# Optimization experiments

Measured on AMD Instinct MI355X. Metric: run time of the kernel, lower is better.

Reference implementation:

```python
import jax, jax.numpy as jnp
import numpy as np


def setup_inputs() -> dict:
    key = jax.random.key(0)
    ks = jax.random.split(key, 8)
    B, T, DIM = 4096, 64, 16
    H1, H2, LAT = 256, 256, 64
    KD = DIM + LAT  # Koopman dim = 80
    x = jax.random.normal(ks[0], (B, T, DIM), dtype=jnp.float32)
    # Encoder: Linear(16->256, bias), Linear(256->256, bias), Linear(256->64, no bias)
    W1 = jax.random.normal(ks[1], (H1, DIM), dtype=jnp.float32) / np.sqrt(DIM)
    b1 = jnp.zeros((H1,), dtype=jnp.float32)
    W2 = jax.random.normal(ks[2], (H2, H1), dtype=jnp.float32) / np.sqrt(H1)
    b2 = jnp.zeros((H2,), dtype=jnp.float32)
    W3 = jax.random.normal(ks[3], (LAT, H2), dtype=jnp.float32) / np.sqrt(H2)
    # Koopman operator, scaled for stable 63-step rollout
    K = jax.random.normal(ks[4], (KD, KD), dtype=jnp.float32) * (0.9 / np.sqrt(KD))
    return {"x": x, "W1": W1, "b1": b1, "W2": W2, "b2": b2, "W3": W3,
            "K": K, "n_shifts": 64}


def reference(x, W1, b1, W2, b2, W3, K, n_shifts):
    # x: [B, T, dim]; slice to n_shifts steps
    x = x[:, :n_shifts, :]
    # Encoder MLP (relu on all but last layer; last layer bias-free, dropout p=0)
    h = jax.nn.relu(jnp.einsum('btd,hd->bth', x, W1) + b1)
    h = jax.nn.relu(jnp.einsum('bth,gh->btg', h, W2) + b2)
    g = jnp.einsum('btg,lg->btl', h, W3)
    y = jnp.concatenate([x, g], axis=-1)  # [B, T, dim+lat]
    # Linear recurrence: y_{n+1} = y_n @ K^T, starting from y[:, 0]
    y0 = y[:, 0, :]  # [B, KD]

    def step(carry, _):
        nxt = carry @ K.T
        return nxt, nxt

    _, rest = jax.lax.scan(step, y0, None, length=n_shifts - 1)  # [T-1, B, KD]
    y_pred = jnp.concatenate([y0[:, None, :], jnp.swapaxes(rest, 0, 1)], axis=1)
    return y, y_pred
```

## Files before the change

### kernel.cpp

```cpp
#include <hip/hip_runtime.h>
#include <hip/hip_bf16.h>

#define NB   4096
#define NT   64
#define NDIM 16
#define NH1  256
#define NH2  256
#define NLAT 64
#define NKD  80
#define YROW (NT * NKD)
#define KTAB 98304
#define KSLOT 15360

#define FROW 184
#define FIMG_B (80 * FROW * 2)

typedef __attribute__((ext_vector_type(8))) short bf16x8;
typedef __attribute__((ext_vector_type(4))) float f32x4;

#define MFMA __builtin_amdgcn_mfma_f32_16x16x32_bf16

static __device__ __forceinline__ short f2bf(float f) {
  union { float f; unsigned u; } v; v.f = f;
  unsigned r = v.u + 0x7fffu + ((v.u >> 16) & 1u);
  return (short)(r >> 16);
}
static __device__ __forceinline__ float bf2f(short h) {
  union { unsigned u; float f; } v; v.u = ((unsigned)(unsigned short)h) << 16;
  return v.f;
}
static __device__ __forceinline__ bf16x8 pack8(float4 a, float4 b) {
  bf16x8 r;
  r[0] = f2bf(a.x); r[1] = f2bf(a.y); r[2] = f2bf(a.z); r[3] = f2bf(a.w);
  r[4] = f2bf(b.x); r[5] = f2bf(b.y); r[6] = f2bf(b.z); r[7] = f2bf(b.w);
  return r;
}
static __device__ __forceinline__ void split8(float4 v0, float4 v1, bf16x8& h, bf16x8& l) {
  h = pack8(v0, v1);
  float4 r0, r1;
  r0.x = v0.x - bf2f(h[0]); r0.y = v0.y - bf2f(h[1]);
  r0.z = v0.z - bf2f(h[2]); r0.w = v0.w - bf2f(h[3]);
  r1.x = v1.x - bf2f(h[4]); r1.y = v1.y - bf2f(h[5]);
  r1.z = v1.z - bf2f(h[6]); r1.w = v1.w - bf2f(h[7]);
  l = pack8(r0, r1);
}

__global__ __launch_bounds__(256) void prep_kernel(const float* __restrict__ W1,
                                                   const float* __restrict__ W2,
                                                   const float* __restrict__ W3,
                                                   short* __restrict__ ws) {
  int i = blockIdx.x * 256 + threadIdx.x;
  {
    int e = i & 7, l = (i >> 3) & 63, nt = (i >> 9) & 15, kk = i >> 13;
    int g = nt * 16 + (l & 15);
    int h = kk * 32 + (l >> 4) * 8 + e;
    ws[i] = f2bf(W2[g * NH1 + h]);
  }
  if (i < 16384) {
    int e = i & 7, l = (i >> 3) & 63, nt = (i >> 9) & 3, kk = i >> 11;
    int g = nt * 16 + (l & 15);
    int h = kk * 32 + (l >> 4) * 8 + e;
    ws[65536 + i] = f2bf(W3[g * NH2 + h]);
  }
  if (i < 8192) {
    int e = i & 7, l = (i >> 3) & 63, nt = i >> 9;
    int g = nt * 16 + (l & 15);
    int k = (l >> 4) * 8 + e;
    ws[81920 + i] = (k < NDIM) ? f2bf(W1[g * NDIM + k]) : (short)0;
  }
}

__global__ void kpow_kernel(const float* __restrict__ Kg, short* __restrict__ ws) {
  extern __shared__ char smem[];
  short* kA   = (short*)smem;
  short* curA = (short*)(smem + FIMG_B);
  short* curB = (short*)(smem + 2 * FIMG_B);
  short* nxtA = (short*)(smem + 3 * FIMG_B);
  short* nxtB = (short*)(smem + 4 * FIMG_B);

  const int tid  = threadIdx.x;
  const int lane = tid & 63;
  const int w    = tid >> 6;
  const int l15  = lane & 15;
  const int kg   = lane >> 4;
  const int t    = blockIdx.x + 1;

  for (int i = tid; i < 6400; i += 512) {
    float v = Kg[i];
    int r = i / 80, c = i - r * 80;
    short hi = f2bf(v);
    short lo = f2bf(v - bf2f(hi));
    kA[r * FROW + c] = hi;        kA[r * FROW + 96 + c] = lo;
    curA[r * FROW + c] = hi;      curA[r * FROW + 96 + c] = lo;
    curB[c * FROW + r] = hi;      curB[c * FROW + 96 + r] = lo;
  }
  __syncthreads();

  auto mm = [&](const short* Ai, const short* Bi, short* DA, short* DB) {
    for (int id = w; id < 25; id += 8) {
      const int mt = id / 5, nt = id % 5;
      f32x4 acc = {0.f, 0.f, 0.f, 0.f};
#pragma unroll
      for (int kk = 0; kk < 3; ++kk) {
        const int k0 = kk * 32 + kg * 8;
        bf16x8 ah = {}, al = {}, bh = {}, bl = {};
        if (k0 < 80) {
          const short* ap = Ai + (mt * 16 + l15) * FROW + k0;
          const short* bp = Bi + (nt * 16 + l15) * FROW + k0;
          ah = *(const bf16x8*)ap;  al = *(const bf16x8*)(ap + 96);
          bh = *(const bf16x8*)bp;  bl = *(const bf16x8*)(bp + 96);
        }
        acc = MFMA(ah, bh, acc, 0, 0, 0);
        acc = MFMA(al, bh, acc, 0, 0, 0);
        acc = MFMA(ah, bl, acc, 0, 0, 0);
      }
      const int n = nt * 16 + l15;
      const int rowb = mt * 16 + kg * 4;
      short4 hs, ls;
#pragma unroll
      for (int r = 0; r < 4; ++r) {
        float v = acc[r];
        short hi = f2bf(v);
        short lo = f2bf(v - bf2f(hi));
        DA[(rowb + r) * FROW + n] = hi;
        DA[(rowb + r) * FROW + 96 + n] = lo;
        ((short*)&hs)[r] = hi;
        ((short*)&ls)[r] = lo;
      }
      *(short4*)(DB + n * FROW + rowb) = hs;
      *(short4*)(DB + n * FROW + 96 + rowb) = ls;
    }
    __syncthreads();
  };

  const int h = 31 - __clz(t);
  for (int bit = h - 1; bit >= 0; --bit) {
    mm(curA, curB, nxtA, nxtB);
    { short* p;
      p = curA; curA = nxtA; nxtA = p;
      p = curB; curB = nxtB; nxtB = p; }
    if ((t >> bit) & 1) {
      mm(kA, curB, nxtA, nxtB);
      { short* p;
        p = curA; curA = nxtA; nxtA = p;
        p = curB; curB = nxtB; nxtB = p; }
    }
  }

  short* kt = ws + KTAB + t * KSLOT;
  for (int s = tid; s < 960; s += 512) {
    int f = s >> 6, ln = s & 63;
    int kk = f / 5, nt = f % 5;
    int k0 = kk * 32 + (ln >> 4) * 8;
    int n  = nt * 16 + (ln & 15);
    bf16x8 h8 = {}, l8 = {};
    if (k0 < 80) {
      const short* ap = curA + n * FROW + k0;
      h8 = *(const bf16x8*)ap;
      l8 = *(const bf16x8*)(ap + 96);
    }
    *(bf16x8*)(kt + f * 512 + ln * 8) = h8;
    *(bf16x8*)(kt + 7680 + f * 512 + ln * 8) = l8;
  }
}

__global__ __launch_bounds__(256, 4) void mlp_kernel(const float* __restrict__ x,
                                                     const float* __restrict__ b1g,
                                                     const float* __restrict__ b2g,
                                                     const short* __restrict__ ws,
                                                     float* __restrict__ y) {
  extern __shared__ char smem[];
  short* h1s = (short*)smem;

  const int tid  = threadIdx.x;
  const int lane = tid & 63;
  const int w    = tid >> 6;
  const int l15  = lane & 15;
  const int kg   = lane >> 4;
  const long b   = blockIdx.x;

  const short* W2f = ws;
  const short* W3f = ws + 65536;
  const short* W1f = ws + 81920;

  const float4 xv = ((const float4*)(x + b * 1024))[tid];

  bf16x8 xf[4];
#pragma unroll
  for (int j = 0; j < 4; ++j) {
    const int tok = j * 16 + l15;
    bf16x8 f = {};
    if (kg < 2) {
      const float4* p = (const float4*)(x + (b * 64 + tok) * 16 + kg * 8);
      f = pack8(p[0], p[1]);
    }
    xf[j] = f;
  }

#pragma unroll
  for (int i = 0; i < 4; ++i) {
    const int mt = w * 4 + i;
    const bf16x8 wa = *(const bf16x8*)(W1f + (mt * 64 + lane) * 8);
    const float4 bias = *(const float4*)(b1g + mt * 16 + kg * 4);
#pragma unroll
    for (int j = 0; j < 4; ++j) {
      f32x4 c = {0.f, 0.f, 0.f, 0.f};
      c = MFMA(wa, xf[j], c, 0, 0, 0);
      const int tok = j * 16 + l15;
      float v0 = c[0] + bias.x; v0 = v0 > 0.f ? v0 : 0.f;
      float v1 = c[1] + bias.y; v1 = v1 > 0.f ? v1 : 0.f;
      float v2 = c[2] + bias.z; v2 = v2 > 0.f ? v2 : 0.f;
      float v3 = c[3] + bias.w; v3 = v3 > 0.f ? v3 : 0.f;
      short4 st = {f2bf(v0), f2bf(v1), f2bf(v2), f2bf(v3)};
      *(short4*)(h1s + tok * 264 + mt * 16 + kg * 4) = st;
    }
  }
  __syncthreads();

  f32x4 acc2[4][4];
#pragma unroll
  for (int i = 0; i < 4; ++i)
#pragma unroll
    for (int j = 0; j < 4; ++j) acc2[i][j] = (f32x4){0.f, 0.f, 0.f, 0.f};

#pragma unroll 2
  for (int kk = 0; kk < 8; ++kk) {
    bf16x8 wa[4], hb[4];
#pragma unroll
    for (int i = 0; i < 4; ++i)
      wa[i] = *(const bf16x8*)(W2f + ((kk * 16 + w * 4 + i) * 64 + lane) * 8);
#pragma unroll
    for (int j = 0; j < 4; ++j)
      hb[j] = *(const bf16x8*)(h1s + (j * 16 + l15) * 264 + kk * 32 + kg * 8);
#pragma unroll
    for (int i = 0; i < 4; ++i)
#pragma unroll
      for (int j = 0; j < 4; ++j)
        acc2[i][j] = MFMA(wa[i], hb[j], acc2[i][j], 0, 0, 0);
  }
  __syncthreads();

#pragma unroll
  for (int i = 0; i < 4; ++i) {
    const int mt = w * 4 + i;
    const float4 bias = *(const float4*)(b2g + mt * 16 + kg * 4);
#pragma unroll
    for (int j = 0; j < 4; ++j) {
      const int tok = j * 16 + l15;
      float v0 = acc2[i][j][0] + bias.x; v0 = v0 > 0.f ? v0 : 0.f;
      float v1 = acc2[i][j][1] + bias.y; v1 = v1 > 0.f ? v1 : 0.f;
      float v2 = acc2[i][j][2] + bias.z; v2 = v2 > 0.f ? v2 : 0.f;
      float v3 = acc2[i][j][3] + bias.w; v3 = v3 > 0.f ? v3 : 0.f;
      short4 st = {f2bf(v0), f2bf(v1), f2bf(v2), f2bf(v3)};
      *(short4*)(h1s + tok * 264 + mt * 16 + kg * 4) = st;
    }
  }
  __syncthreads();

  f32x4 acc3[4];
#pragma unroll
  for (int j = 0; j < 4; ++j) acc3[j] = (f32x4){0.f, 0.f, 0.f, 0.f};
#pragma unroll 2
  for (int kk = 0; kk < 8; ++kk) {
    const bf16x8 wa = *(const bf16x8*)(W3f + ((kk * 4 + w) * 64 + lane) * 8);
#pragma unroll
    for (int j = 0; j < 4; ++j) {
      const bf16x8 hb =
          *(const bf16x8*)(h1s + (j * 16 + l15) * 264 + kk * 32 + kg * 8);
      acc3[j] = MFMA(wa, hb, acc3[j], 0, 0, 0);
    }
  }

  *(float4*)(y + (b * 64 + (tid >> 2)) * 80 + (tid & 3) * 4) = xv;
#pragma unroll
  for (int j = 0; j < 4; ++j) {
    const int tok = j * 16 + l15;
    *(float4*)(y + (b * 64 + tok) * 80 + 16 + w * 16 + kg * 4) =
        *(float4*)&acc3[j];
  }
}

__global__ __launch_bounds__(512, 4) void ypred_kernel(const short* __restrict__ ws,
                                                       const float* __restrict__ y,
                                                       float* __restrict__ yp) {
  const int tid  = threadIdx.x;
  const int lane = tid & 63;
  const int w    = tid >> 6;
  const int m16  = lane & 15;
  const int kg   = lane >> 4;
  const int bc   = blockIdx.x & 15;
  const int t    = blockIdx.x >> 4;
  const long b0  = (long)bc * 256;

  if (t == 0) {
    for (int i = tid; i < 5120; i += 512) {
      int r = i / 20, q = (i % 20) * 4;
      *(float4*)(yp + (b0 + r) * YROW + q) = *(const float4*)(y + (b0 + r) * YROW + q);
    }
    return;
  }

  bf16x8 ah[2][3], al[2][3];
#pragma unroll
  for (int m = 0; m < 2; ++m) {
#pragma unroll
    for (int kk = 0; kk < 3; ++kk) {
      const int k0 = kk * 32 + kg * 8;
      bf16x8 fh = {}, fl = {};
      if (k0 < 80) {
        const float4* p =
            (const float4*)(y + (b0 + (2 * w + m) * 16 + m16) * YROW + k0);
        split8(p[0], p[1], fh, fl);
      }
      ah[m][kk] = fh;
      al[m][kk] = fl;
    }
  }

  const short* kt = ws + KTAB + t * KSLOT;
  f32x4 acc[2][5];
#pragma unroll
  for (int m = 0; m < 2; ++m)
#pragma unroll
    for (int nt = 0; nt < 5; ++nt) acc[m][nt] = (f32x4){0.f, 0.f, 0.f, 0.f};

#pragma unroll
  for (int kk = 0; kk < 3; ++kk) {
#pragma unroll
    for (int nt = 0; nt < 5; ++nt) {
      const bf16x8 bh = *(const bf16x8*)(kt + ((kk * 5 + nt) * 64 + lane) * 8);
      const bf16x8 bl = *(const bf16x8*)(kt + 7680 + ((kk * 5 + nt) * 64 + lane) * 8);
#pragma unroll
      for (int m = 0; m < 2; ++m) {
        acc[m][nt] = MFMA(ah[m][kk], bh, acc[m][nt], 0, 0, 0);
        acc[m][nt] = MFMA(al[m][kk], bh, acc[m][nt], 0, 0, 0);
        acc[m][nt] = MFMA(ah[m][kk], bl, acc[m][nt], 0, 0, 0);
      }
    }
  }
#pragma unroll
  for (int m = 0; m < 2; ++m)
#pragma unroll
    for (int nt = 0; nt < 5; ++nt)
#pragma unroll
      for (int r = 0; r < 4; ++r)
        yp[(b0 + (2 * w + m) * 16 + kg * 4 + r) * YROW + (long)t * 80 + nt * 16 + m16] =
            acc[m][nt][r];
}

extern "C" void kernel_launch(void* const* d_in, const int* in_sizes, int n_in,
                              void* d_out, int out_size, void* d_ws, size_t ws_size,
                              hipStream_t stream) {
  const float* x  = (const float*)d_in[0];
  const float* W1 = (const float*)d_in[1];
  const float* b1 = (const float*)d_in[2];
  const float* W2 = (const float*)d_in[3];
  const float* b2 = (const float*)d_in[4];
  const float* W3 = (const float*)d_in[5];
  const float* Kg = (const float*)d_in[6];
  float* y  = (float*)d_out;
  float* yp = y + (long)NB * YROW;
  short* ws = (short*)d_ws;

  prep_kernel<<<256, 256, 0, stream>>>(W1, W2, W3, ws);
  kpow_kernel<<<63, 512, 5 * FIMG_B, stream>>>(Kg, ws);
  mlp_kernel<<<NB, 256, 33792, stream>>>(x, b1, b2, ws, y);
  ypred_kernel<<<16 * 64, 512, 0, stream>>>(ws, y, yp);
}
```

Baseline: 118.7 us.

## Switch encoder MLP to 32x32x16 MFMA tiles with prefetched operands

Rewrites the encoder MLP kernel and weight packing to use 32x32x16 bf16 MFMA instead of 16x16x32. Each wave covers larger output tiles with fewer instructions, and the layer-1 pass no longer pads the 16-wide input to 32. The layer-2 loop now software-prefetches the next weight and activation fragments. Shared memory becomes static. The larger tiles use more accumulator registers per wave, which could reduce occupancy.

```diff
diff --git a/kernel.cpp b/kernel.cpp
--- a/kernel.cpp
+++ b/kernel.cpp
@@ -15,10 +15,12 @@
 #define FROW 184
 #define FIMG_B (80 * FROW * 2)
 
-typedef __attribute__((ext_vector_type(8))) short bf16x8;
-typedef __attribute__((ext_vector_type(4))) float f32x4;
-
-#define MFMA __builtin_amdgcn_mfma_f32_16x16x32_bf16
+typedef __attribute__((ext_vector_type(8)))  short bf16x8;
+typedef __attribute__((ext_vector_type(4)))  float f32x4;
+typedef __attribute__((ext_vector_type(16))) float f32x16;
+
+#define MFMA   __builtin_amdgcn_mfma_f32_16x16x32_bf16
+#define MFMA32 __builtin_amdgcn_mfma_f32_32x32x16_bf16
 
 static __device__ __forceinline__ short f2bf(float f) {
   union { float f; unsigned u; } v; v.f = f;
@@ -51,22 +53,22 @@
                                                    short* __restrict__ ws) {
   int i = blockIdx.x * 256 + threadIdx.x;
   {
-    int e = i & 7, l = (i >> 3) & 63, nt = (i >> 9) & 15, kk = i >> 13;
-    int g = nt * 16 + (l & 15);
-    int h = kk * 32 + (l >> 4) * 8 + e;
-    ws[i] = f2bf(W2[g * NH1 + h]);
+    int e = i & 7, l = (i >> 3) & 63, mt = (i >> 9) & 7, kk = i >> 12;
+    int g = mt * 32 + (l & 31);
+    int k = kk * 16 + (l >> 5) * 8 + e;
+    ws[i] = f2bf(W2[g * NH1 + k]);
   }
   if (i < 16384) {
-    int e = i & 7, l = (i >> 3) & 63, nt = (i >> 9) & 3, kk = i >> 11;
-    int g = nt * 16 + (l & 15);
-    int h = kk * 32 + (l >> 4) * 8 + e;
-    ws[65536 + i] = f2bf(W3[g * NH2 + h]);
-  }
-  if (i < 8192) {
-    int e = i & 7, l = (i >> 3) & 63, nt = i >> 9;
-    int g = nt * 16 + (l & 15);
-    int k = (l >> 4) * 8 + e;
-    ws[81920 + i] = (k < NDIM) ? f2bf(W1[g * NDIM + k]) : (short)0;
+    int e = i & 7, l = (i >> 3) & 63, mt = (i >> 9) & 1, kk = i >> 10;
+    int g = mt * 32 + (l & 31);
+    int k = kk * 16 + (l >> 5) * 8 + e;
+    ws[65536 + i] = f2bf(W3[g * NH2 + k]);
+  }
+  if (i < 4096) {
+    int e = i & 7, l = (i >> 3) & 63, mt = i >> 9;
+    int g = mt * 32 + (l & 31);
+    int k = (l >> 5) * 8 + e;
+    ws[81920 + i] = f2bf(W1[g * NDIM + k]);
   }
 }
 
@@ -169,14 +171,13 @@
                                                      const float* __restrict__ b2g,
                                                      const short* __restrict__ ws,
                                                      float* __restrict__ y) {
-  extern __shared__ char smem[];
-  short* h1s = (short*)smem;
+  __shared__ short h1s[64 * 264];
 
   const int tid  = threadIdx.x;
   const int lane = tid & 63;
   const int w    = tid >> 6;
-  const int l15  = lane & 15;
-  const int kg   = lane >> 4;
+  const int l31  = lane & 31;
+  const int hi   = lane >> 5;
   const long b   = blockIdx.x;
 
   const short* W2f = ws;
@@ -185,98 +186,99 @@
 
   const float4 xv = ((const float4*)(x + b * 1024))[tid];
 
-  bf16x8 xf[4];
-#pragma unroll
-  for (int j = 0; j < 4; ++j) {
-    const int tok = j * 16 + l15;
-    bf16x8 f = {};
-    if (kg < 2) {
-      const float4* p = (const float4*)(x + (b * 64 + tok) * 16 + kg * 8);
-      f = pack8(p[0], p[1]);
-    }
-    xf[j] = f;
-  }
-
-#pragma unroll
-  for (int i = 0; i < 4; ++i) {
-    const int mt = w * 4 + i;
-    const bf16x8 wa = *(const bf16x8*)(W1f + (mt * 64 + lane) * 8);
-    const float4 bias = *(const float4*)(b1g + mt * 16 + kg * 4);
-#pragma unroll
-    for (int j = 0; j < 4; ++j) {
-      f32x4 c = {0.f, 0.f, 0.f, 0.f};
-      c = MFMA(wa, xf[j], c, 0, 0, 0);
-      const int tok = j * 16 + l15;
-      float v0 = c[0] + bias.x; v0 = v0 > 0.f ? v0 : 0.f;
-      float v1 = c[1] + bias.y; v1 = v1 > 0.f ? v1 : 0.f;
-      float v2 = c[2] + bias.z; v2 = v2 > 0.f ? v2 : 0.f;
-      float v3 = c[3] + bias.w; v3 = v3 > 0.f ? v3 : 0.f;
-      short4 st = {f2bf(v0), f2bf(v1), f2bf(v2), f2bf(v3)};
-      *(short4*)(h1s + tok * 264 + mt * 16 + kg * 4) = st;
+  bf16x8 xf0, xf1;
+  {
+    const float4* p0 = (const float4*)(x + (b * 64 + l31) * 16 + hi * 8);
+    const float4* p1 = (const float4*)(x + (b * 64 + 32 + l31) * 16 + hi * 8);
+    xf0 = pack8(p0[0], p0[1]);
+    xf1 = pack8(p1[0], p1[1]);
+  }
+
+#pragma unroll
+  for (int i = 0; i < 2; ++i) {
+    const int mt = 2 * w + i;
+    const bf16x8 wa = *(const bf16x8*)(W1f + mt * 512 + lane * 8);
+#pragma unroll
+    for (int nt = 0; nt < 2; ++nt) {
+      f32x16 c = {};
+      c = MFMA32(wa, nt ? xf1 : xf0, c, 0, 0, 0);
+      const int tok = nt * 32 + l31;
+#pragma unroll
+      for (int q = 0; q < 4; ++q) {
+        const int rowb = mt * 32 + q * 8 + 4 * hi;
+        const float4 bias = *(const float4*)(b1g + rowb);
+        float v0 = c[q * 4 + 0] + bias.x; v0 = v0 > 0.f ? v0 : 0.f;
+        float v1 = c[q * 4 + 1] + bias.y; v1 = v1 > 0.f ? v1 : 0.f;
+        float v2 = c[q * 4 + 2] + bias.z; v2 = v2 > 0.f ? v2 : 0.f;
+        float v3 = c[q * 4 + 3] + bias.w; v3 = v3 > 0.f ? v3 : 0.f;
+        short4 st = {f2bf(v0), f2bf(v1), f2bf(v2), f2bf(v3)};
+        *(short4*)(h1s + tok * 264 + rowb) = st;
+      }
     }
   }
   __syncthreads();
 
-  f32x4 acc2[4][4];
-#pragma unroll
-  for (int i = 0; i < 4; ++i)
-#pragma unroll
-    for (int j = 0; j < 4; ++j) acc2[i][j] = (f32x4){0.f, 0.f, 0.f, 0.f};
-
-#pragma unroll 2
-  for (int kk = 0; kk < 8; ++kk) {
-    bf16x8 wa[4], hb[4];
-#pragma unroll
-    for (int i = 0; i < 4; ++i)
-      wa[i] = *(const bf16x8*)(W2f + ((kk * 16 + w * 4 + i) * 64 + lane) * 8);
-#pragma unroll
-    for (int j = 0; j < 4; ++j)
-      hb[j] = *(const bf16x8*)(h1s + (j * 16 + l15) * 264 + kk * 32 + kg * 8);
-#pragma unroll
-    for (int i = 0; i < 4; ++i)
-#pragma unroll
-      for (int j = 0; j < 4; ++j)
-        acc2[i][j] = MFMA(wa[i], hb[j], acc2[i][j], 0, 0, 0);
+  f32x16 acc2[2][2] = {};
+  bf16x8 wa0, wa1, hb0, hb1, wan0, wan1, hbn0, hbn1;
+  wa0 = *(const bf16x8*)(W2f + (2 * w) * 512 + lane * 8);
+  wa1 = *(const bf16x8*)(W2f + (2 * w + 1) * 512 + lane * 8);
+  hb0 = *(const bf16x8*)(h1s + l31 * 264 + hi * 8);
+  hb1 = *(const bf16x8*)(h1s + (32 + l31) * 264 + hi * 8);
+#pragma unroll
+  for (int kk = 0; kk < 16; ++kk) {
+    if (kk < 15) {
+      const short* wb = W2f + ((kk + 1) * 8 + 2 * w) * 512 + lane * 8;
+      wan0 = *(const bf16x8*)wb;
+      wan1 = *(const bf16x8*)(wb + 512);
+      const int co = (kk + 1) * 16 + hi * 8;
+      hbn0 = *(const bf16x8*)(h1s + l31 * 264 + co);
+      hbn1 = *(const bf16x8*)(h1s + (32 + l31) * 264 + co);
+    }
+    acc2[0][0] = MFMA32(wa0, hb0, acc2[0][0], 0, 0, 0);
+    acc2[0][1] = MFMA32(wa0, hb1, acc2[0][1], 0, 0, 0);
+    acc2[1][0] = MFMA32(wa1, hb0, acc2[1][0], 0, 0, 0);
+    acc2[1][1] = MFMA32(wa1, hb1, acc2[1][1], 0, 0, 0);
+    wa0 = wan0; wa1 = wan1; hb0 = hbn0; hb1 = hbn1;
   }
   __syncthreads();
 
 #pragma unroll
-  for (int i = 0; i < 4; ++i) {
-    const int mt = w * 4 + i;
-    const float4 bias = *(const float4*)(b2g + mt * 16 + kg * 4);
-#pragma unroll
-    for (int j = 0; j < 4; ++j) {
-      const int tok = j * 16 + l15;
-      float v0 = acc2[i][j][0] + bias.x; v0 = v0 > 0.f ? v0 : 0.f;
-      float v1 = acc2[i][j][1] + bias.y; v1 = v1 > 0.f ? v1 : 0.f;
-      float v2 = acc2[i][j][2] + bias.z; v2 = v2 > 0.f ? v2 : 0.f;
-      float v3 = acc2[i][j][3] + bias.w; v3 = v3 > 0.f ? v3 : 0.f;
-      short4 st = {f2bf(v0), f2bf(v1), f2bf(v2), f2bf(v3)};
-      *(short4*)(h1s + tok * 264 + mt * 16 + kg * 4) = st;
+  for (int i = 0; i < 2; ++i) {
+    const int mt = 2 * w + i;
+#pragma unroll
+    for (int nt = 0; nt < 2; ++nt) {
+      const int tok = nt * 32 + l31;
+#pragma unroll
+      for (int q = 0; q < 4; ++q) {
+        const int rowb = mt * 32 + q * 8 + 4 * hi;
+        const float4 bias = *(const float4*)(b2g + rowb);
+        float v0 = acc2[i][nt][q * 4 + 0] + bias.x; v0 = v0 > 0.f ? v0 : 0.f;
+        float v1 = acc2[i][nt][q * 4 + 1] + bias.y; v1 = v1 > 0.f ? v1 : 0.f;
+        float v2 = acc2[i][nt][q * 4 + 2] + bias.z; v2 = v2 > 0.f ? v2 : 0.f;
+        float v3 = acc2[i][nt][q * 4 + 3] + bias.w; v3 = v3 > 0.f ? v3 : 0.f;
+        short4 st = {f2bf(v0), f2bf(v1), f2bf(v2), f2bf(v3)};
+        *(short4*)(h1s + tok * 264 + rowb) = st;
+      }
     }
   }
   __syncthreads();
 
-  f32x4 acc3[4];
-#pragma unroll
-  for (int j = 0; j < 4; ++j) acc3[j] = (f32x4){0.f, 0.f, 0.f, 0.f};
-#pragma unroll 2
-  for (int kk = 0; kk < 8; ++kk) {
-    const bf16x8 wa = *(const bf16x8*)(W3f + ((kk * 4 + w) * 64 + lane) * 8);
-#pragma unroll
-    for (int j = 0; j < 4; ++j) {
-      const bf16x8 hb =
-          *(const bf16x8*)(h1s + (j * 16 + l15) * 264 + kk * 32 + kg * 8);
-      acc3[j] = MFMA(wa, hb, acc3[j], 0, 0, 0);
-    }
+  const int mt3 = w & 1;
+  const int nt3 = w >> 1;
+  const int tok3 = nt3 * 32 + l31;
+  f32x16 acc3 = {};
+#pragma unroll
+  for (int kk = 0; kk < 16; ++kk) {
+    const bf16x8 wa = *(const bf16x8*)(W3f + (kk * 2 + mt3) * 512 + lane * 8);
+    const bf16x8 hb = *(const bf16x8*)(h1s + tok3 * 264 + kk * 16 + hi * 8);
+    acc3 = MFMA32(wa, hb, acc3, 0, 0, 0);
   }
 
   *(float4*)(y + (b * 64 + (tid >> 2)) * 80 + (tid & 3) * 4) = xv;
 #pragma unroll
-  for (int j = 0; j < 4; ++j) {
-    const int tok = j * 16 + l15;
-    *(float4*)(y + (b * 64 + tok) * 80 + 16 + w * 16 + kg * 4) =
-        *(float4*)&acc3[j];
+  for (int q = 0; q < 4; ++q) {
+    float4 st = {acc3[q * 4 + 0], acc3[q * 4 + 1], acc3[q * 4 + 2], acc3[q * 4 + 3]};
+    *(float4*)(y + (b * 64 + tok3) * 80 + 16 + mt3 * 32 + q * 8 + 4 * hi) = st;
   }
 }
 
@@ -364,6 +366,6 @@
 
   prep_kernel<<<256, 256, 0, stream>>>(W1, W2, W3, ws);
   kpow_kernel<<<63, 512, 5 * FIMG_B, stream>>>(Kg, ws);
-  mlp_kernel<<<NB, 256, 33792, stream>>>(x, b1, b2, ws, y);
+  mlp_kernel<<<NB, 256, 0, stream>>>(x, b1, b2, ws, y);
   ypred_kernel<<<16 * 64, 512, 0, stream>>>(ws, y, yp);
 }
```

Result: slower. 129.5 us (+9.1%).

## Compute y0 in a small pre-pass and fuse MLP with y_pred rollout blocks

Applied to the files above, without the earlier changes.

A small kernel first encodes only the t=0 token of every batch into a workspace buffer. A single fused launch then interleaves MLP blocks (two of every three) with y_pred blocks (one of every three), and the y_pred blocks read y0 from that workspace instead of from the full y output. This removes the serial dependency between the MLP kernel and the rollout kernel, so the rollout's large output writes can overlap with the MLP compute and one launch boundary goes away. In exchange the y0 tokens are encoded twice, and y_pred blocks drop to 256 threads, which changes their per-block work split.

```diff
diff --git a/kernel.cpp b/kernel.cpp
--- a/kernel.cpp
+++ b/kernel.cpp
@@ -11,6 +11,7 @@
 #define YROW (NT * NKD)
 #define KTAB 98304
 #define KSLOT 15360
+#define Y0OFF 1081344
 
 #define FROW 184
 #define FIMG_B (80 * FROW * 2)
@@ -164,26 +165,24 @@
   }
 }
 
-__global__ __launch_bounds__(256, 4) void mlp_kernel(const float* __restrict__ x,
-                                                     const float* __restrict__ b1g,
-                                                     const float* __restrict__ b2g,
-                                                     const short* __restrict__ ws,
-                                                     float* __restrict__ y) {
-  extern __shared__ char smem[];
-  short* h1s = (short*)smem;
-
-  const int tid  = threadIdx.x;
+template <int XSTRIDE, int OROW>
+static __device__ __forceinline__ void mlp_body(long b, const float* __restrict__ x,
+                                                const float* __restrict__ b1g,
+                                                const float* __restrict__ b2g,
+                                                const short* __restrict__ ws,
+                                                float* __restrict__ yo, short* h1s,
+                                                int tid) {
   const int lane = tid & 63;
   const int w    = tid >> 6;
   const int l15  = lane & 15;
   const int kg   = lane >> 4;
-  const long b   = blockIdx.x;
 
   const short* W2f = ws;
   const short* W3f = ws + 65536;
   const short* W1f = ws + 81920;
 
-  const float4 xv = ((const float4*)(x + b * 1024))[tid];
+  const float4 xv =
+      *(const float4*)(x + (b * 64 + (tid >> 2)) * XSTRIDE + (tid & 3) * 4);
 
   bf16x8 xf[4];
 #pragma unroll
@@ -191,7 +190,7 @@
     const int tok = j * 16 + l15;
     bf16x8 f = {};
     if (kg < 2) {
-      const float4* p = (const float4*)(x + (b * 64 + tok) * 16 + kg * 8);
+      const float4* p = (const float4*)(x + (b * 64 + tok) * XSTRIDE + kg * 8);
       f = pack8(p[0], p[1]);
     }
     xf[j] = f;
@@ -271,31 +270,39 @@
     }
   }
 
-  *(float4*)(y + (b * 64 + (tid >> 2)) * 80 + (tid & 3) * 4) = xv;
+  *(float4*)(yo + (b * 64 + (tid >> 2)) * OROW + (tid & 3) * 4) = xv;
 #pragma unroll
   for (int j = 0; j < 4; ++j) {
     const int tok = j * 16 + l15;
-    *(float4*)(y + (b * 64 + tok) * 80 + 16 + w * 16 + kg * 4) =
+    *(float4*)(yo + (b * 64 + tok) * OROW + 16 + w * 16 + kg * 4) =
         *(float4*)&acc3[j];
   }
 }
 
-__global__ __launch_bounds__(512, 4) void ypred_kernel(const short* __restrict__ ws,
-                                                       const float* __restrict__ y,
-                                                       float* __restrict__ yp) {
-  const int tid  = threadIdx.x;
+__global__ __launch_bounds__(256, 4) void mlp0_kernel(const float* __restrict__ x,
+                                                      const float* __restrict__ b1g,
+                                                      const float* __restrict__ b2g,
+                                                      short* __restrict__ ws) {
+  __shared__ short h1s[64 * 264];
+  float* y0t = (float*)(ws + Y0OFF);
+  mlp_body<1024, 80>((long)blockIdx.x, x, b1g, b2g, ws, y0t, h1s, threadIdx.x);
+}
+
+static __device__ __forceinline__ void ypred_body(int g, const short* __restrict__ ws,
+                                                  float* __restrict__ yp, int tid) {
   const int lane = tid & 63;
   const int w    = tid >> 6;
   const int m16  = lane & 15;
   const int kg   = lane >> 4;
-  const int bc   = blockIdx.x & 15;
-  const int t    = blockIdx.x >> 4;
-  const long b0  = (long)bc * 256;
+  const int bc   = g & 31;
+  const int t    = g >> 5;
+  const long b0  = (long)bc * 128;
+  const float* y0t = (const float*)(ws + Y0OFF);
 
   if (t == 0) {
-    for (int i = tid; i < 5120; i += 512) {
+    for (int i = tid; i < 2560; i += 256) {
       int r = i / 20, q = (i % 20) * 4;
-      *(float4*)(yp + (b0 + r) * YROW + q) = *(const float4*)(y + (b0 + r) * YROW + q);
+      *(float4*)(yp + (b0 + r) * YROW + q) = *(const float4*)(y0t + (b0 + r) * 80 + q);
     }
     return;
   }
@@ -309,7 +316,7 @@
       bf16x8 fh = {}, fl = {};
       if (k0 < 80) {
         const float4* p =
-            (const float4*)(y + (b0 + (2 * w + m) * 16 + m16) * YROW + k0);
+            (const float4*)(y0t + (b0 + (2 * w + m) * 16 + m16) * 80 + k0);
         split8(p[0], p[1], fh, fl);
       }
       ah[m][kk] = fh;
@@ -346,6 +353,24 @@
       for (int r = 0; r < 4; ++r)
         yp[(b0 + (2 * w + m) * 16 + kg * 4 + r) * YROW + (long)t * 80 + nt * 16 + m16] =
             acc[m][nt][r];
+}
+
+__global__ __launch_bounds__(256, 4) void fused_kernel(const float* __restrict__ x,
+                                                       const float* __restrict__ b1g,
+                                                       const float* __restrict__ b2g,
+                                                       const short* __restrict__ ws,
+                                                       float* __restrict__ y,
+                                                       float* __restrict__ yp) {
+  extern __shared__ char smem[];
+  const int bid = blockIdx.x;
+  const int g = bid / 3;
+  const int r = bid - 3 * g;
+  if (r == 2) {
+    ypred_body(g, ws, yp, threadIdx.x);
+  } else {
+    mlp_body<16, 80>((long)(g * 2 + r), x, b1g, b2g, ws, y, (short*)smem,
+                     threadIdx.x);
+  }
 }
 
 extern "C" void kernel_launch(void* const* d_in, const int* in_sizes, int n_in,
@@ -364,6 +389,6 @@
 
   prep_kernel<<<256, 256, 0, stream>>>(W1, W2, W3, ws);
   kpow_kernel<<<63, 512, 5 * FIMG_B, stream>>>(Kg, ws);
-  mlp_kernel<<<NB, 256, 33792, stream>>>(x, b1, b2, ws, y);
-  ypred_kernel<<<16 * 64, 512, 0, stream>>>(ws, y, yp);
-}
+  mlp0_kernel<<<64, 256, 0, stream>>>(x, b1, b2, ws);
+  fused_kernel<<<6144, 256, 64 * 264 * 2, stream>>>(x, b1, b2, ws, y, yp);
+}
```

New measurement: 127.1 us. +7.1%, slower.
